# Kernel optimization log

Hardware: AMD Instinct MI355X
Metric: run time of the kernel (lower is better)

Reference implementation:

```python
import jax, jax.numpy as jnp
import numpy as np

DIM = 2048
H = 16           # n_heads
KV = 4           # n_kv_heads
G = H // KV      # gqa factor
CQ = 128         # q_compressed_dim
QN, QR = 96, 32  # q nope / rope head dims
CKV = 128        # kv_compressed_dim
KN, KR = 64, 64  # k nope / rope head dims
VD = 256         # v_head_dim
THETA = 10000.0


def _t5_layer_norm(x, gamma, eps=1e-5):
    mu = jnp.mean(x, axis=-1, keepdims=True)
    var = jnp.var(x, axis=-1, keepdims=True)
    return (x - mu) * jax.lax.rsqrt(var + eps) * gamma


def _rope(x):
    # x: [B, H, S, D] with interleaved even/odd rotation, positions = arange(S)
    S, D = x.shape[-2], x.shape[-1]
    inv_freq = 1.0 / THETA ** (jnp.arange(0, D, 2, dtype=jnp.float32) / D)
    ang = jnp.arange(S, dtype=jnp.float32)[:, None] * inv_freq  # [S, D/2]
    cos = jnp.cos(ang).astype(x.dtype)
    sin = jnp.sin(ang).astype(x.dtype)
    xe, xo = x[..., ::2], x[..., 1::2]
    re = xe * cos - xo * sin
    ro = xe * sin + xo * cos
    return jnp.stack((re, ro), axis=-1).reshape(x.shape)


def setup_inputs() -> dict:
    key = jax.random.key(0)
    ks = jax.random.split(key, 7)
    s = 0.02
    return {
        "x": jax.random.normal(ks[0], (2, 2048, DIM), dtype=jnp.float32),
        "w_dq": jax.random.normal(ks[1], (DIM, CQ), dtype=jnp.float32) * s,
        "gamma_q": jnp.ones((CQ,), dtype=jnp.float32),
        "w_uq": jax.random.normal(ks[2], (CQ, H * (QN + QR)), dtype=jnp.float32) * s,
        "w_dkv": jax.random.normal(ks[3], (DIM, CKV + KR), dtype=jnp.float32) * s,
        "gamma_kv": jnp.ones((CKV,), dtype=jnp.float32),
        "w_ukv": jax.random.normal(ks[4], (CKV, KV * (KN + VD)), dtype=jnp.float32) * s,
        "w_o": jax.random.normal(ks[5], (H * VD, DIM), dtype=jnp.float32) * s,
    }


def reference(x, w_dq, gamma_q, w_uq, w_dkv, gamma_kv, w_ukv, w_o):
    B, S, _ = x.shape
    # low-rank Q path
    cq = _t5_layer_norm(x @ w_dq, gamma_q)                     # [B,S,CQ]
    q = cq @ w_uq                                              # [B,S,H*(QN+QR)]
    q_nope = q[..., : H * QN].reshape(B, S, H, QN).transpose(0, 2, 1, 3)
    q_rope = q[..., H * QN :].reshape(B, S, H, QR).transpose(0, 2, 1, 3)
    q_rope = _rope(q_rope)
    q_states = jnp.concatenate((q_nope, q_rope), axis=-1)      # [B,H,S,QN+QR]

    # low-rank KV path + decoupled shared rope key
    ckv_kr = x @ w_dkv                                         # [B,S,CKV+KR]
    ckv = _t5_layer_norm(ckv_kr[..., :CKV], gamma_kv)
    k_rope = _rope(ckv_kr[..., CKV:][:, None, :, :])           # [B,1,S,KR]
    kv = ckv @ w_ukv                                           # [B,S,KV*(KN+VD)]
    k_nope = kv[..., : KV * KN].reshape(B, S, KV, KN).transpose(0, 2, 1, 3)
    v_states = kv[..., KV * KN :].reshape(B, S, KV, VD).transpose(0, 2, 1, 3)
    k_states = jnp.concatenate(
        (k_nope, jnp.broadcast_to(k_rope, (B, KV, S, KR))), axis=-1
    )                                                          # [B,KV,S,KN+KR]

    # grouped-query attention: broadcast kv heads instead of materializing repeats
    dqk = QN + QR  # == KN + KR == 128
    qg = q_states.reshape(B, KV, G, S, dqk)
    scores = jnp.einsum("bgrqd,bgkd->bgrqk", qg, k_states) / jnp.sqrt(
        jnp.asarray(dqk, dtype=x.dtype)
    )
    causal = jnp.triu(jnp.ones((S, S), dtype=bool), k=1)
    scores = jnp.where(causal, -jnp.inf, scores)
    attn = jax.nn.softmax(scores, axis=-1)
    out = jnp.einsum("bgrqk,bgkv->bgrqv", attn, v_states)      # [B,KV,G,S,VD]
    out = out.reshape(B, H, S, VD).transpose(0, 2, 1, 3).reshape(B, S, H * VD)
    return out @ w_o
```

## Files before the change

### kernel.cpp

```cpp
#include <hip/hip_runtime.h>
#include <hip/hip_bf16.h>
#include <math.h>

#define DIM   2048
#define S_LEN 2048
#define BATCH 2
#define NH    16
#define NKV   4
#define CQ_   128
#define QN_   96
#define QR_   32
#define CKV_  128
#define KN_   64
#define KR_   64
#define VD_   256
#define DQK   192
#define DV    128
#define ROWS_TOT (BATCH*S_LEN)
#define QK_SCALE 0.08838834764831845f
#define LOG2E    1.4426950408889634f

typedef __attribute__((ext_vector_type(8)))  short short8;
typedef __attribute__((ext_vector_type(4)))  short short4v;
typedef __attribute__((ext_vector_type(4)))  float float4v;
typedef __attribute__((ext_vector_type(16))) float float16v;
typedef __attribute__((ext_vector_type(4)))  int   int4v;

__device__ inline short f2bf(float x) {
    union { __hip_bfloat16 h; short s; } u;
    u.h = __float2bfloat16(x);
    return u.s;
}

__device__ __forceinline__ void gl_lds16(const short* g, short* lds) {
    __builtin_amdgcn_global_load_lds(
        (const __attribute__((address_space(1))) unsigned int*)(g),
        (__attribute__((address_space(3))) unsigned int*)(lds),
        16, 0, 0);
}

__device__ __forceinline__ short8 cast8(const float* p) {
    float4 a = *reinterpret_cast<const float4*>(p);
    float4 b = *reinterpret_cast<const float4*>(p + 4);
    short8 o;
    o[0] = f2bf(a.x); o[1] = f2bf(a.y); o[2] = f2bf(a.z); o[3] = f2bf(a.w);
    o[4] = f2bf(b.x); o[5] = f2bf(b.y); o[6] = f2bf(b.z); o[7] = f2bf(b.w);
    return o;
}

__global__ __launch_bounds__(256)
void kw_prep(const float* __restrict__ w_o, const float* __restrict__ w_uq,
             const float* __restrict__ w_ukv, const float* __restrict__ w_dq,
             const float* __restrict__ w_dkv,
             short* __restrict__ wdT, short* __restrict__ w_uqT,
             short* __restrict__ WqcombT, short* __restrict__ WcombT,
             float* __restrict__ tq, float* __restrict__ tk)
{
    __shared__ char smem[67584];
    const int bid = blockIdx.x, tid = threadIdx.x;
    const int lane = tid & 63, wid = tid >> 6;
    const int g = lane >> 4, l15 = lane & 15;

    if (bid < 224) {
        float* tf = (float*)smem;
        int lb, nct, R; short* dst;
        if (bid < 160) { lb = bid;       nct = 5;  R = 2048; dst = wdT;   }
        else           { lb = bid - 160; nct = 32; R = 128;  dst = w_uqT; }
        const int ct = lb % nct, rt = lb / nct;
        const int r0 = rt * 64, c0 = ct * 64;
        const float* src; int stride, nbase;
        if (bid < 160) {
            if (ct < 2) { src = w_dq;  stride = 128; nbase = c0; }
            else        { src = w_dkv; stride = 192; nbase = c0 - 128; }
        } else { src = w_uq; stride = 2048; nbase = c0; }

        #pragma unroll
        for (int u4 = 0; u4 < 4; ++u4) {
            int u = u4 * 256 + tid;
            int kr = u >> 4, nc = (u & 15) * 4;
            float4 v = *reinterpret_cast<const float4*>(&src[(size_t)(r0 + kr) * stride + nbase + nc]);
            tf[kr * 65 + nc + 0] = v.x; tf[kr * 65 + nc + 1] = v.y;
            tf[kr * 65 + nc + 2] = v.z; tf[kr * 65 + nc + 3] = v.w;
        }
        __syncthreads();
        #pragma unroll
        for (int u2 = 0; u2 < 2; ++u2) {
            int u = u2 * 256 + tid;
            int nr = u >> 3, kc8 = (u & 7) * 8;
            short8 o;
            #pragma unroll
            for (int j = 0; j < 8; ++j) o[j] = f2bf(tf[(kc8 + j) * 65 + nr]);
            *reinterpret_cast<short8*>(&dst[(size_t)(c0 + nr) * R + r0 + kc8]) = o;
        }
        return;
    }
    if (bid < 608) {
        int gid = (bid - 224) * 256 + tid;
        int spos = gid / 48, e = gid - spos * 48;
        if (e < 16) {
            float inv = powf(10000.f, -(float)(2 * e) / 32.f);
            float sn, c; sincosf((float)spos * inv, &sn, &c);
            tq[(spos * 16 + e) * 2 + 0] = c;
            tq[(spos * 16 + e) * 2 + 1] = sn;
        } else {
            int i2 = e - 16;
            float inv = powf(10000.f, -(float)(2 * i2) / 64.f);
            float sn, c; sincosf((float)spos * inv, &sn, &c);
            tk[(spos * 32 + i2) * 2 + 0] = c;
            tk[(spos * 32 + i2) * 2 + 1] = sn;
        }
        return;
    }
    if (bid < 624) {
        const int h = bid - 608, kvh = h >> 2;
        float4v acc[2][8];
        #pragma unroll
        for (int mi = 0; mi < 2; ++mi)
            #pragma unroll
            for (int nj = 0; nj < 8; ++nj) acc[mi][nj] = (float4v){0.f, 0.f, 0.f, 0.f};
        #pragma unroll
        for (int kb = 0; kb < 2; ++kb) {
            short8 af[2], bf[8];
            #pragma unroll
            for (int mi = 0; mi < 2; ++mi) {
                int j = wid * 32 + mi * 16 + l15;
                af[mi] = cast8(&w_ukv[(size_t)j * 1280 + kvh * 64 + kb * 32 + g * 8]);
            }
            #pragma unroll
            for (int nj = 0; nj < 8; ++nj) {
                int e = nj * 16 + l15;
                bf[nj] = cast8(&w_uq[(size_t)e * 2048 + h * 96 + kb * 32 + g * 8]);
            }
            #pragma unroll
            for (int mi = 0; mi < 2; ++mi)
                #pragma unroll
                for (int nj = 0; nj < 8; ++nj)
                    acc[mi][nj] = __builtin_amdgcn_mfma_f32_16x16x32_bf16(
                        af[mi], bf[nj], acc[mi][nj], 0, 0, 0);
        }
        #pragma unroll
        for (int mi = 0; mi < 2; ++mi)
            #pragma unroll
            for (int nj = 0; nj < 8; ++nj)
                #pragma unroll
                for (int r = 0; r < 4; ++r)
                    WqcombT[(size_t)h * 16384 + (wid * 32 + mi * 16 + g * 4 + r) * 128
                            + nj * 16 + l15] = f2bf(acc[mi][nj][r]);
        return;
    }

    {
        const int bb = bid - 624;
        const int h = bb >> 4, nt = bb & 15, kvh = h >> 2;
        const int wm = wid >> 1, wn = wid & 1;
        short* wot = (short*)smem;

        for (int u = tid; u < 8192; u += 256) {
            int r = u >> 5, c4 = (u & 31) * 4;
            float4 v = *reinterpret_cast<const float4*>(
                &w_o[(size_t)(h * 256 + r) * DIM + nt * 128 + c4]);
            wot[(c4 + 0) * 264 + r] = f2bf(v.x);
            wot[(c4 + 1) * 264 + r] = f2bf(v.y);
            wot[(c4 + 2) * 264 + r] = f2bf(v.z);
            wot[(c4 + 3) * 264 + r] = f2bf(v.w);
        }
        __syncthreads();

        float4v acc[4][4];
        #pragma unroll
        for (int mi = 0; mi < 4; ++mi)
            #pragma unroll
            for (int nj = 0; nj < 4; ++nj) acc[mi][nj] = (float4v){0.f, 0.f, 0.f, 0.f};
        for (int kb = 0; kb < 8; ++kb) {
            short8 af[4], bf[4];
            #pragma unroll
            for (int mi = 0; mi < 4; ++mi) {
                int nl = wm * 64 + mi * 16 + l15;
                af[mi] = *reinterpret_cast<const short8*>(
                    &wot[nl * 264 + kb * 32 + g * 8]);
            }
            #pragma unroll
            for (int nj = 0; nj < 4; ++nj) {
                int c = wn * 64 + nj * 16 + l15;
                bf[nj] = cast8(&w_ukv[(size_t)c * 1280 + 256 + kvh * 256 + kb * 32 + g * 8]);
            }
            #pragma unroll
            for (int mi = 0; mi < 4; ++mi)
                #pragma unroll
                for (int nj = 0; nj < 4; ++nj)
                    acc[mi][nj] = __builtin_amdgcn_mfma_f32_16x16x32_bf16(
                        af[mi], bf[nj], acc[mi][nj], 0, 0, 0);
        }
        #pragma unroll
        for (int mi = 0; mi < 4; ++mi)
            #pragma unroll
            for (int nj = 0; nj < 4; ++nj)
                #pragma unroll
                for (int r = 0; r < 4; ++r)
                    WcombT[(size_t)(nt * 128 + wm * 64 + mi * 16 + g * 4 + r) * 2048
                           + h * 128 + wn * 64 + nj * 16 + l15] = f2bf(acc[mi][nj][r]);
    }
}

__global__ __launch_bounds__(256)
void k12_mfma(const float* __restrict__ x, const short* __restrict__ wdT,
              const float* __restrict__ gamma_q, const float* __restrict__ gamma_kv,
              const float* __restrict__ tk, const float* __restrict__ tq,
              const short* __restrict__ WqcombT, const short* __restrict__ w_uqT,
              short* __restrict__ kimg, short* __restrict__ vimg,
              short* __restrict__ q_states)
{
    __shared__ float ys[16][321];
    __shared__ float st[16][4];
    __shared__ short cqs[16][136];
    const int tid = threadIdx.x, lane = tid & 63, w = tid >> 6;
    const int g = lane >> 4, l15 = lane & 15;
    const int m0 = blockIdx.x * 16;
    const int wn0 = w * 80;

    float4v acc5[5];
    #pragma unroll
    for (int nj = 0; nj < 5; ++nj) acc5[nj] = (float4v){0.f, 0.f, 0.f, 0.f};

    const float* arow = x + (size_t)(m0 + l15) * 2048 + g * 8;
    for (int ks = 0; ks < 64; ++ks) {
        short8 a = cast8(arow + ks * 32);
        #pragma unroll
        for (int nj = 0; nj < 5; ++nj) {
            short8 bf = *reinterpret_cast<const short8*>(
                wdT + (size_t)(wn0 + nj * 16 + l15) * 2048 + ks * 32 + g * 8);
            acc5[nj] = __builtin_amdgcn_mfma_f32_16x16x32_bf16(a, bf, acc5[nj], 0, 0, 0);
        }
    }

    #pragma unroll
    for (int nj = 0; nj < 5; ++nj)
        #pragma unroll
        for (int r = 0; r < 4; ++r)
            ys[g * 4 + r][wn0 + nj * 16 + l15] = acc5[nj][r];
    __syncthreads();

    if (tid < 32) {
        int row = tid >> 1, seg = tid & 1, base = seg * 128;
        float s1 = 0.f, s2 = 0.f;
        for (int j = 0; j < 128; ++j) { float v = ys[row][base + j]; s1 += v; s2 += v * v; }
        float mu  = s1 * (1.f / 128.f);
        float var = s2 * (1.f / 128.f) - mu * mu;
        st[row][seg * 2 + 0] = mu;
        st[row][seg * 2 + 1] = rsqrtf(var + 1e-5f);
    }
    __syncthreads();

    for (int i = tid; i < 16 * 128; i += 256) {
        int row = i >> 7, col = i & 127;
        cqs[row][col] =
            f2bf((ys[row][col] - st[row][0]) * st[row][1] * gamma_q[col] * (QK_SCALE * LOG2E));
    }
    for (int i = tid; i < 16 * 192; i += 256) {
        int row = i / 192, d = i - row * 192;
        int r = m0 + row, b = r >> 11, spos = r & (S_LEN - 1);
        int tile = b * 32 + (spos >> 6);
        if (d < 128) {
            float val = (ys[row][128 + d] - st[row][2]) * st[row][3] * gamma_kv[d];
            short v_ = f2bf(val);
            size_t vslot = (d >> 5) * 256 + ((spos >> 5) & 1) * 128
                           + ((spos >> 4) & 1) * 64 + ((spos >> 3) & 1) * 32 + (d & 31);
            vimg[((size_t)tile * 1024 + vslot) * 8 + (spos & 7)] = v_;
            size_t kslot = ((spos >> 5) & 1) * 768 + (d >> 4) * 64
                           + ((d >> 3) & 1) * 32 + (spos & 31);
            kimg[((size_t)tile * 1536 + kslot) * 8 + (d & 7)] = v_;
        } else {
            int dd = d - 128, i2 = dd >> 1;
            float xe = ys[row][256 + (dd & ~1)];
            float xo = ys[row][256 + (dd | 1)];
            float c  = tk[(spos * 32 + i2) * 2 + 0];
            float sn = tk[(spos * 32 + i2) * 2 + 1];
            float val = (dd & 1) ? (xe * sn + xo * c) : (xe * c - xo * sn);
            size_t kslot = ((spos >> 5) & 1) * 768 + (d >> 4) * 64
                           + ((d >> 3) & 1) * 32 + (spos & 31);
            kimg[((size_t)tile * 1536 + kslot) * 8 + (d & 7)] = f2bf(val);
        }
    }
    __syncthreads();

    short8 af[4];
    #pragma unroll
    for (int ks = 0; ks < 4; ++ks)
        af[ks] = *reinterpret_cast<const short8*>(&cqs[l15][ks * 32 + g * 8]);

    for (int ns = 0; ns < 3; ++ns) {
        const int nb = ns * 1024 + w * 256;
        float4v acc[16];
        #pragma unroll
        for (int nj = 0; nj < 16; ++nj) acc[nj] = (float4v){0.f, 0.f, 0.f, 0.f};

        #pragma unroll
        for (int ks = 0; ks < 4; ++ks)
            #pragma unroll
            for (int nj = 0; nj < 16; ++nj) {
                int j = nb + nj * 16 + l15;
                int h = j / 192, t = j - h * 192;
                const short* brow;
                if (t < 128)       brow = WqcombT + (size_t)h * 16384 + (size_t)t * 128;
                else if (t < 160)  brow = w_uqT + (size_t)(h * 96 + 64 + (t - 128)) * 128;
                else               brow = w_uqT + (size_t)(1536 + h * 32 + (t - 160)) * 128;
                short8 bf = *reinterpret_cast<const short8*>(brow + ks * 32 + g * 8);
                acc[nj] = __builtin_amdgcn_mfma_f32_16x16x32_bf16(af[ks], bf, acc[nj], 0, 0, 0);
            }

        #pragma unroll
        for (int nj = 0; nj < 16; ++nj) {
            int j = nb + nj * 16 + l15;
            int h = j / 192, t = j - h * 192;
            if (t < 160) {
                #pragma unroll
                for (int r = 0; r < 4; ++r) {
                    int rg = m0 + g * 4 + r, bb = rg >> 11, spos = rg & (S_LEN - 1);
                    q_states[((size_t)(bb * NH + h) * S_LEN + spos) * DQK + t] =
                        f2bf(acc[nj][r]);
                }
            } else {
                int dd = t - 160, i2 = dd >> 1;
                #pragma unroll
                for (int r = 0; r < 4; ++r) {
                    int rg = m0 + g * 4 + r, bb = rg >> 11, spos = rg & (S_LEN - 1);
                    float v = acc[nj][r];
                    float p = __shfl_xor(v, 1, 64);
                    float c  = tq[(spos * 16 + i2) * 2 + 0];
                    float sn = tq[(spos * 16 + i2) * 2 + 1];
                    float out = (dd & 1) ? (p * sn + v * c) : (v * c - p * sn);
                    q_states[((size_t)(bb * NH + h) * S_LEN + spos) * DQK + t] = f2bf(out);
                }
            }
        }
    }
}

__global__ __launch_bounds__(512, 1)
void k4_attn_mfma(const short* __restrict__ q_states,
                  const short* __restrict__ kimg,
                  const short* __restrict__ vimg,
                  short* __restrict__ attn_out)
{
    __shared__ __align__(16) short ks_lds[3][12288];
    __shared__ __align__(16) short vt_lds[2][8192];

    const int tid = threadIdx.x, lane = tid & 63, w = tid >> 6;
    const int bid = blockIdx.x;
    const int l31 = lane & 31, hi = lane >> 5;
    const int g = w & 3, h = w >> 2;
    const int qt = (bid < 256) ? (15 - (bid >> 5)) : (7 - ((bid - 256) >> 5));
    const int bh = bid & 31;
    const int h_head = bh & 15, b = bh >> 4;

    const short* kfbase = kimg + (size_t)b * 32 * 12288;
    const short* vfbase = vimg + (size_t)b * 32 * 8192;

    const int qrow0 = qt * 128 + g * 32;
    const int qglob = qrow0 + l31;

    short8 qcur[12];
    {
        const short* qr = q_states +
            ((size_t)(b * NH + h_head) * S_LEN + qglob) * DQK + hi * 8;
        #pragma unroll
        for (int st = 0; st < 12; ++st)
            qcur[st] = *reinterpret_cast<const short8*>(qr + st * 16);
    }

    float16v o[4];
    #pragma unroll
    for (int dt = 0; dt < 4; ++dt)
        #pragma unroll
        for (int r = 0; r < 16; ++r) o[dt][r] = 0.f;
    float mreg = -1e30f, lreg = 0.f;

    const int nkt = 2 * (qt + 1);

    auto issueK = [&](int kt, int bufi) {
        const short* src = kfbase + (size_t)kt * 12288;
        #pragma unroll
        for (int i = 0; i < 3; ++i) {
            int c = w * 3 + i;
            gl_lds16(src + c * 512 + lane * 8, &ks_lds[bufi][c * 512]);
        }
    };
    auto issueV = [&](int kt, int bufi) {
        const short* src = vfbase + (size_t)kt * 8192;
        #pragma unroll
        for (int i = 0; i < 2; ++i) {
            int c = w * 2 + i;
            gl_lds16(src + c * 512 + lane * 8, &vt_lds[bufi][c * 512]);
        }
    };

    issueK(0, 0);
    issueV(0, 0);
    issueK(1, 1);

    for (int seq = 0; seq < nkt; ++seq) {
        if (seq < nkt - 1) { asm volatile("s_waitcnt vmcnt(3)" ::: "memory"); }
        else               { asm volatile("s_waitcnt vmcnt(0)" ::: "memory"); }
        __builtin_amdgcn_s_barrier();
        __builtin_amdgcn_sched_barrier(0);

        if (seq + 1 < nkt) issueV(seq + 1, (seq + 1) & 1);
        if (seq + 2 < nkt) issueK(seq + 2, (seq + 2) % 3);

        const int kvb = seq * 64 + h * 32;
        if (kvb <= qrow0 + 31) {
            const short* kbuf = &ks_lds[seq % 3][h * 6144];
            float16v sa, sb;
            #pragma unroll
            for (int r = 0; r < 16; ++r) { sa[r] = 0.f; sb[r] = 0.f; }
            __builtin_amdgcn_s_setprio(1);
            #pragma unroll
            for (int st = 0; st < 12; st += 2) {
                short8 kf0 = *reinterpret_cast<const short8*>(kbuf + st * 512 + lane * 8);
                sa = __builtin_amdgcn_mfma_f32_32x32x16_bf16(kf0, qcur[st], sa, 0, 0, 0);
                short8 kf1 = *reinterpret_cast<const short8*>(kbuf + (st + 1) * 512 + lane * 8);
                sb = __builtin_amdgcn_mfma_f32_32x32x16_bf16(kf1, qcur[st + 1], sb, 0, 0, 0);
            }
            __builtin_amdgcn_s_setprio(0);
            float16v s;
            #pragma unroll
            for (int r = 0; r < 16; ++r) s[r] = sa[r] + sb[r];

            if (kvb + 31 > qrow0) {
                #pragma unroll
                for (int r = 0; r < 16; ++r) {
                    int kc = kvb + ((r & 3) + 8 * (r >> 2) + 4 * hi);
                    if (kc > qglob) s[r] = -1e30f;
                }
            }

            float mx = s[0];
            #pragma unroll
            for (int r = 1; r < 16; ++r) mx = fmaxf(mx, s[r]);
            mx = fmaxf(mx, __shfl_xor(mx, 32, 64));
            bool need = mx > mreg + 8.f;
            if (__ballot(need)) {
                float mnew = fmaxf(mreg, mx);
                float corr = exp2f(mreg - mnew);
                mreg = mnew;
                lreg *= corr;
                #pragma unroll
                for (int dt = 0; dt < 4; ++dt)
                    #pragma unroll
                    for (int r = 0; r < 16; ++r) o[dt][r] *= corr;
            }
            #pragma unroll
            for (int r = 0; r < 16; ++r) s[r] = exp2f(s[r] - mreg);
            float ps = 0.f;
            #pragma unroll
            for (int r = 0; r < 16; ++r) ps += s[r];
            ps += __shfl_xor(ps, 32, 64);
            lreg += ps;

            const short* vbuf = &vt_lds[seq & 1][h * 1024];
            __builtin_amdgcn_s_setprio(1);
            #pragma unroll
            for (int ks = 0; ks < 2; ++ks) {
                const int rb = ks * 8;
                int c01, c23, c45, c67;
                asm("v_cvt_pk_bf16_f32 %0, %1, %2" : "=v"(c01) : "v"(s[rb+0]), "v"(s[rb+1]));
                asm("v_cvt_pk_bf16_f32 %0, %1, %2" : "=v"(c23) : "v"(s[rb+2]), "v"(s[rb+3]));
                asm("v_cvt_pk_bf16_f32 %0, %1, %2" : "=v"(c45) : "v"(s[rb+4]), "v"(s[rb+5]));
                asm("v_cvt_pk_bf16_f32 %0, %1, %2" : "=v"(c67) : "v"(s[rb+6]), "v"(s[rb+7]));
                asm("v_permlane32_swap_b32 %0, %1" : "+v"(c01), "+v"(c45));
                asm("v_permlane32_swap_b32 %0, %1" : "+v"(c23), "+v"(c67));
                union { int4v i4; short8 s8; } u_;
                u_.i4.x = c01; u_.i4.y = c23; u_.i4.z = c45; u_.i4.w = c67;
                short8 pa = u_.s8;
                #pragma unroll
                for (int dt = 0; dt < 4; ++dt) {
                    short8 vf = *reinterpret_cast<const short8*>(
                        vbuf + dt * 2048 + ks * 512 + lane * 8);
                    o[dt] = __builtin_amdgcn_mfma_f32_32x32x16_bf16(vf, pa, o[dt], 0, 0, 0);
                }
            }
            __builtin_amdgcn_s_setprio(0);
        }
    }

    __syncthreads();
    {
        float* mlb = (float*)(&ks_lds[0][0]);
        mlb[w * 64 + lane] = mreg;
        mlb[512 + w * 64 + lane] = lreg;
    }
    __syncthreads();
    float s0f = 0.f, s1f = 0.f;
    if (h == 0) {
        float* mlb = (float*)(&ks_lds[0][0]);
        float m1 = mlb[(w + 4) * 64 + lane];
        float l1 = mlb[512 + (w + 4) * 64 + lane];
        float ms = fmaxf(mreg, m1);
        float c0 = exp2f(mreg - ms), c1 = exp2f(m1 - ms);
        float ls = lreg * c0 + l1 * c1;
        s0f = c0 / ls; s1f = c1 / ls;
    }
    float* cb = (float*)(&ks_lds[0][0]) + 1024;
    short* obase = attn_out + ((size_t)(b * S_LEN + qglob)) * 2048 + h_head * 128;
    for (int dt = 0; dt < 4; ++dt) {
        __syncthreads();
        if (h == 1) {
            #pragma unroll
            for (int r = 0; r < 16; ++r)
                cb[r * 256 + g * 64 + lane] = o[dt][r];
        }
        __syncthreads();
        if (h == 0) {
            #pragma unroll
            for (int r = 0; r < 16; ++r)
                o[dt][r] = o[dt][r] * s0f + cb[r * 256 + g * 64 + lane] * s1f;
            #pragma unroll
            for (int k4i = 0; k4i < 4; ++k4i) {
                int d0 = dt * 32 + k4i * 8 + hi * 4;
                short4v pk;
                #pragma unroll
                for (int j = 0; j < 4; ++j) pk[j] = f2bf(o[dt][k4i * 4 + j]);
                *reinterpret_cast<short4v*>(obase + d0) = pk;
            }
        }
    }
}

__global__ __launch_bounds__(256)
void k5_gemm_mfma(const short* __restrict__ A,
                  const short* __restrict__ Bt,
                  float* __restrict__ C)
{
    __shared__ __align__(16) short at[128 * 64];
    __shared__ __align__(16) short bt[128 * 64];
    const int tid  = threadIdx.x;
    const int lane = tid & 63;
    const int wid  = tid >> 6;
    const int wm = wid >> 1, wn = wid & 1;
    const int g = lane >> 4, l15 = lane & 15;
    const int wg = (blockIdx.x & 7) * 64 + (blockIdx.x >> 3);
    const int bn = wg & 15, bm = wg >> 4;
    const int m0 = bm * 128, n0 = bn * 128;

    float4v acc[4][4];
    #pragma unroll
    for (int mi = 0; mi < 4; ++mi)
        #pragma unroll
        for (int nj = 0; nj < 4; ++nj) acc[mi][nj] = (float4v){0.f, 0.f, 0.f, 0.f};

    for (int k0 = 0; k0 < 2048; k0 += 64) {
        __syncthreads();
        #pragma unroll
        for (int i = 0; i < 4; ++i) {
            int row = wid * 32 + i * 8 + (lane >> 3);
            int ch  = lane & 7;
            gl_lds16(A + (size_t)(m0 + row) * 2048 + k0 + ((ch ^ (row & 7)) * 8),
                     at + wid * 2048 + i * 512);
            gl_lds16(Bt + (size_t)(n0 + row) * 2048 + k0 + ((ch ^ (row & 7)) * 8),
                     bt + wid * 2048 + i * 512);
        }
        __syncthreads();

        #pragma unroll
        for (int kb = 0; kb < 2; ++kb) {
            short8 af[4], bfr[4];
            #pragma unroll
            for (int mi = 0; mi < 4; ++mi) {
                int row = wm * 64 + mi * 16 + l15;
                af[mi] = *reinterpret_cast<const short8*>(
                    at + row * 64 + (((g + 4 * kb) ^ (row & 7)) * 8));
            }
            #pragma unroll
            for (int nj = 0; nj < 4; ++nj) {
                int row = wn * 64 + nj * 16 + l15;
                bfr[nj] = *reinterpret_cast<const short8*>(
                    bt + row * 64 + (((g + 4 * kb) ^ (row & 7)) * 8));
            }
            #pragma unroll
            for (int mi = 0; mi < 4; ++mi)
                #pragma unroll
                for (int nj = 0; nj < 4; ++nj)
                    acc[mi][nj] = __builtin_amdgcn_mfma_f32_16x16x32_bf16(
                        af[mi], bfr[nj], acc[mi][nj], 0, 0, 0);
        }
    }

    #pragma unroll
    for (int mi = 0; mi < 4; ++mi)
        #pragma unroll
        for (int nj = 0; nj < 4; ++nj)
            #pragma unroll
            for (int r = 0; r < 4; ++r)
                C[(size_t)(m0 + wm * 64 + mi * 16 + g * 4 + r) * DIM + n0 + wn * 64 + nj * 16 + l15] =
                    acc[mi][nj][r];
}

extern "C" void kernel_launch(void* const* d_in, const int* in_sizes, int n_in,
                              void* d_out, int out_size, void* d_ws, size_t ws_size,
                              hipStream_t stream)
{
    const float* x        = (const float*)d_in[0];
    const float* w_dq     = (const float*)d_in[1];
    const float* gamma_q  = (const float*)d_in[2];
    const float* w_uq     = (const float*)d_in[3];
    const float* w_dkv    = (const float*)d_in[4];
    const float* gamma_kv = (const float*)d_in[5];
    const float* w_ukv    = (const float*)d_in[6];
    const float* w_o      = (const float*)d_in[7];
    float* out = (float*)d_out;

    char* ws = (char*)d_ws;
    float* tq       = (float*)(ws);
    float* tk       = (float*)(ws + (1ull  << 20));
    short* w_uqT    = (short*)(ws + (2ull  << 20));
    short* wdT      = (short*)(ws + (3ull  << 20));
    short* WqcombT  = (short*)(ws + (5ull  << 20));
    short* kimg     = (short*)(ws + (6ull  << 20));
    short* vimg     = (short*)(ws + (8ull  << 20));
    short* q_states = (short*)(ws + (10ull << 20));
    short* attn_out = (short*)(ws + (36ull << 20));
    short* WcombT   = (short*)(ws + (52ull << 20));

    kw_prep<<<dim3(880), dim3(256), 0, stream>>>(
        w_o, w_uq, w_ukv, w_dq, w_dkv, wdT, w_uqT, WqcombT, WcombT, tq, tk);

    k12_mfma<<<dim3(ROWS_TOT / 16), dim3(256), 0, stream>>>(
        x, wdT, gamma_q, gamma_kv, tk, tq, WqcombT, w_uqT, kimg, vimg, q_states);

    k4_attn_mfma<<<dim3(512), dim3(512), 0, stream>>>(
        q_states, kimg, vimg, attn_out);

    k5_gemm_mfma<<<dim3(512), dim3(256), 0, stream>>>(
        attn_out, WcombT, out);
}
```

Measured before the change: 252.4 us.

## Split fused down-projection/up-projection kernel into two kernels for more parallelism

```diff
diff --git a/kernel.cpp b/kernel.cpp
--- a/kernel.cpp
+++ b/kernel.cpp
@@ -203,24 +203,22 @@
 }
 
 __global__ __launch_bounds__(256)
-void k12_mfma(const float* __restrict__ x, const short* __restrict__ wdT,
-              const float* __restrict__ gamma_q, const float* __restrict__ gamma_kv,
-              const float* __restrict__ tk, const float* __restrict__ tq,
-              const short* __restrict__ WqcombT, const short* __restrict__ w_uqT,
-              short* __restrict__ kimg, short* __restrict__ vimg,
-              short* __restrict__ q_states)
+void k1_mfma(const float* __restrict__ x, const short* __restrict__ wdT,
+             const float* __restrict__ gamma_q, const float* __restrict__ gamma_kv,
+             const float* __restrict__ tk,
+             short* __restrict__ cq_bf, short* __restrict__ kimg,
+             short* __restrict__ vimg)
 {
     __shared__ float ys[16][321];
     __shared__ float st[16][4];
-    __shared__ short cqs[16][136];
     const int tid = threadIdx.x, lane = tid & 63, w = tid >> 6;
     const int g = lane >> 4, l15 = lane & 15;
     const int m0 = blockIdx.x * 16;
     const int wn0 = w * 80;
 
-    float4v acc5[5];
-    #pragma unroll
-    for (int nj = 0; nj < 5; ++nj) acc5[nj] = (float4v){0.f, 0.f, 0.f, 0.f};
+    float4v acc[5];
+    #pragma unroll
+    for (int nj = 0; nj < 5; ++nj) acc[nj] = (float4v){0.f, 0.f, 0.f, 0.f};
 
     const float* arow = x + (size_t)(m0 + l15) * 2048 + g * 8;
     for (int ks = 0; ks < 64; ++ks) {
@@ -229,7 +227,7 @@
         for (int nj = 0; nj < 5; ++nj) {
             short8 bf = *reinterpret_cast<const short8*>(
                 wdT + (size_t)(wn0 + nj * 16 + l15) * 2048 + ks * 32 + g * 8);
-            acc5[nj] = __builtin_amdgcn_mfma_f32_16x16x32_bf16(a, bf, acc5[nj], 0, 0, 0);
+            acc[nj] = __builtin_amdgcn_mfma_f32_16x16x32_bf16(a, bf, acc[nj], 0, 0, 0);
         }
     }
 
@@ -237,7 +235,7 @@
     for (int nj = 0; nj < 5; ++nj)
         #pragma unroll
         for (int r = 0; r < 4; ++r)
-            ys[g * 4 + r][wn0 + nj * 16 + l15] = acc5[nj][r];
+            ys[g * 4 + r][wn0 + nj * 16 + l15] = acc[nj][r];
     __syncthreads();
 
     if (tid < 32) {
@@ -253,7 +251,8 @@
 
     for (int i = tid; i < 16 * 128; i += 256) {
         int row = i >> 7, col = i & 127;
-        cqs[row][col] =
+        int r = m0 + row;
+        cq_bf[(size_t)r * CQ_ + col] =
             f2bf((ys[row][col] - st[row][0]) * st[row][1] * gamma_q[col] * (QK_SCALE * LOG2E));
     }
     for (int i = tid; i < 16 * 192; i += 256) {
@@ -281,56 +280,65 @@
             kimg[((size_t)tile * 1536 + kslot) * 8 + (d & 7)] = f2bf(val);
         }
     }
-    __syncthreads();
+}
+
+__global__ __launch_bounds__(256)
+void k2_mfma(const short* __restrict__ cq_bf, const short* __restrict__ WqcombT,
+             const short* __restrict__ w_uqT, const float* __restrict__ tq,
+             short* __restrict__ q_states)
+{
+    const int tid = threadIdx.x, lane = tid & 63, w = tid >> 6;
+    const int g = lane >> 4, l15 = lane & 15;
+    const int bm = blockIdx.x / 3, ns = blockIdx.x % 3;
+    const int m0 = bm * 16;
+    const int nb = ns * 1024 + w * 256;
 
     short8 af[4];
     #pragma unroll
     for (int ks = 0; ks < 4; ++ks)
-        af[ks] = *reinterpret_cast<const short8*>(&cqs[l15][ks * 32 + g * 8]);
-
-    for (int ns = 0; ns < 3; ++ns) {
-        const int nb = ns * 1024 + w * 256;
-        float4v acc[16];
-        #pragma unroll
-        for (int nj = 0; nj < 16; ++nj) acc[nj] = (float4v){0.f, 0.f, 0.f, 0.f};
-
-        #pragma unroll
-        for (int ks = 0; ks < 4; ++ks)
-            #pragma unroll
-            for (int nj = 0; nj < 16; ++nj) {
-                int j = nb + nj * 16 + l15;
-                int h = j / 192, t = j - h * 192;
-                const short* brow;
-                if (t < 128)       brow = WqcombT + (size_t)h * 16384 + (size_t)t * 128;
-                else if (t < 160)  brow = w_uqT + (size_t)(h * 96 + 64 + (t - 128)) * 128;
-                else               brow = w_uqT + (size_t)(1536 + h * 32 + (t - 160)) * 128;
-                short8 bf = *reinterpret_cast<const short8*>(brow + ks * 32 + g * 8);
-                acc[nj] = __builtin_amdgcn_mfma_f32_16x16x32_bf16(af[ks], bf, acc[nj], 0, 0, 0);
-            }
-
+        af[ks] = *reinterpret_cast<const short8*>(
+            cq_bf + (size_t)(m0 + l15) * 128 + ks * 32 + g * 8);
+
+    float4v acc[16];
+    #pragma unroll
+    for (int nj = 0; nj < 16; ++nj) acc[nj] = (float4v){0.f, 0.f, 0.f, 0.f};
+
+    #pragma unroll
+    for (int ks = 0; ks < 4; ++ks)
         #pragma unroll
         for (int nj = 0; nj < 16; ++nj) {
             int j = nb + nj * 16 + l15;
             int h = j / 192, t = j - h * 192;
-            if (t < 160) {
-                #pragma unroll
-                for (int r = 0; r < 4; ++r) {
-                    int rg = m0 + g * 4 + r, bb = rg >> 11, spos = rg & (S_LEN - 1);
-                    q_states[((size_t)(bb * NH + h) * S_LEN + spos) * DQK + t] =
-                        f2bf(acc[nj][r]);
-                }
-            } else {
-                int dd = t - 160, i2 = dd >> 1;
-                #pragma unroll
-                for (int r = 0; r < 4; ++r) {
-                    int rg = m0 + g * 4 + r, bb = rg >> 11, spos = rg & (S_LEN - 1);
-                    float v = acc[nj][r];
-                    float p = __shfl_xor(v, 1, 64);
-                    float c  = tq[(spos * 16 + i2) * 2 + 0];
-                    float sn = tq[(spos * 16 + i2) * 2 + 1];
-                    float out = (dd & 1) ? (p * sn + v * c) : (v * c - p * sn);
-                    q_states[((size_t)(bb * NH + h) * S_LEN + spos) * DQK + t] = f2bf(out);
-                }
+            const short* brow;
+            if (t < 128)       brow = WqcombT + (size_t)h * 16384 + (size_t)t * 128;
+            else if (t < 160)  brow = w_uqT + (size_t)(h * 96 + 64 + (t - 128)) * 128;
+            else               brow = w_uqT + (size_t)(1536 + h * 32 + (t - 160)) * 128;
+            short8 bf = *reinterpret_cast<const short8*>(brow + ks * 32 + g * 8);
+            acc[nj] = __builtin_amdgcn_mfma_f32_16x16x32_bf16(af[ks], bf, acc[nj], 0, 0, 0);
+        }
+
+    #pragma unroll
+    for (int nj = 0; nj < 16; ++nj) {
+        int j = nb + nj * 16 + l15;
+        int h = j / 192, t = j - h * 192;
+        if (t < 160) {
+            #pragma unroll
+            for (int r = 0; r < 4; ++r) {
+                int rg = m0 + g * 4 + r, bb = rg >> 11, spos = rg & (S_LEN - 1);
+                q_states[((size_t)(bb * NH + h) * S_LEN + spos) * DQK + t] =
+                    f2bf(acc[nj][r]);
+            }
+        } else {
+            int dd = t - 160, i2 = dd >> 1;
+            #pragma unroll
+            for (int r = 0; r < 4; ++r) {
+                int rg = m0 + g * 4 + r, bb = rg >> 11, spos = rg & (S_LEN - 1);
+                float v = acc[nj][r];
+                float p = __shfl_xor(v, 1, 64);
+                float c  = tq[(spos * 16 + i2) * 2 + 0];
+                float sn = tq[(spos * 16 + i2) * 2 + 1];
+                float out = (dd & 1) ? (p * sn + v * c) : (v * c - p * sn);
+                q_states[((size_t)(bb * NH + h) * S_LEN + spos) * DQK + t] = f2bf(out);
             }
         }
     }
@@ -617,6 +625,7 @@
     short* WqcombT  = (short*)(ws + (5ull  << 20));
     short* kimg     = (short*)(ws + (6ull  << 20));
     short* vimg     = (short*)(ws + (8ull  << 20));
+    short* cq_bf    = (short*)(ws + (9ull  << 20));
     short* q_states = (short*)(ws + (10ull << 20));
     short* attn_out = (short*)(ws + (36ull << 20));
     short* WcombT   = (short*)(ws + (52ull << 20));
@@ -624,8 +633,11 @@
     kw_prep<<<dim3(880), dim3(256), 0, stream>>>(
         w_o, w_uq, w_ukv, w_dq, w_dkv, wdT, w_uqT, WqcombT, WcombT, tq, tk);
 
-    k12_mfma<<<dim3(ROWS_TOT / 16), dim3(256), 0, stream>>>(
-        x, wdT, gamma_q, gamma_kv, tk, tq, WqcombT, w_uqT, kimg, vimg, q_states);
+    k1_mfma<<<dim3(ROWS_TOT / 16), dim3(256), 0, stream>>>(
+        x, wdT, gamma_q, gamma_kv, tk, cq_bf, kimg, vimg);
+
+    k2_mfma<<<dim3((ROWS_TOT / 16) * 3), dim3(256), 0, stream>>>(
+        cq_bf, WqcombT, w_uqT, tq, q_states);
 
     k4_attn_mfma<<<dim3(512), dim3(512), 0, stream>>>(
         q_states, kimg, vimg, attn_out);
```

Result: faster. 240.4 us (-4.8%).
